# Kernel optimization log

Hardware: AMD Instinct MI355X
Metric: run time of the kernel (lower is better)

Reference implementation:

```python
import jax, jax.numpy as jnp
import numpy as np

TYPE_PANEL, TYPE_DIALOG, TYPE_CHAR = 1, 2, 3
NUM_ELEMS = 64  # max element index per type (panel count cap per page)
B, S, D = 8, 4096, 768
NPC, NDS = 4, 4  # num_panel_classes, num_dialog_shapes


def setup_inputs() -> dict:
    key = jax.random.key(0)
    ks = jax.random.split(key, 16)
    w = lambda k, shp: jax.random.normal(k, shp, dtype=jnp.float32) * 0.02
    return {
        "element_types": jax.random.randint(ks[0], (B, S), 0, 4, dtype=jnp.int32),
        "element_indices": jax.random.randint(ks[1], (B, S), 0, NUM_ELEMS, dtype=jnp.int32),
        "parent_panel_indices": jax.random.randint(ks[2], (B, S), 0, NUM_ELEMS, dtype=jnp.int32),
        "style_vector": jax.random.normal(ks[3], (B, 4), dtype=jnp.float32),
        "type_emb": w(ks[4], (4, D)),
        "index_emb": w(ks[5], (NUM_ELEMS, D)),
        "parent_emb": w(ks[6], (NUM_ELEMS, D)),
        "style_w": w(ks[7], (4, D)),
        "style_b": jnp.zeros((D,), jnp.float32),
        "ln_g": jnp.ones((D,), jnp.float32),
        "ln_b": jnp.zeros((D,), jnp.float32),
        "panel_w": w(ks[8], (D, NPC + 4)),
        "panel_b": jnp.zeros((NPC + 4,), jnp.float32),
        "dialog_w": w(ks[9], (2 * D, NDS + 4)),
        "dialog_b": jnp.zeros((NDS + 4,), jnp.float32),
        "char_w": w(ks[10], (2 * D, 4)),
        "char_b": jnp.zeros((4,), jnp.float32),
    }


def reference(element_types, element_indices, parent_panel_indices, style_vector,
              type_emb, index_emb, parent_emb, style_w, style_b, ln_g, ln_b,
              panel_w, panel_b, dialog_w, dialog_b, char_w, char_b):
    Bv, Sv = element_types.shape
    # --- TokenLayoutEncoder: embedding sum + style projection + LayerNorm ---
    x = type_emb[element_types] + index_emb[element_indices] + parent_emb[parent_panel_indices]
    x = x + (style_vector @ style_w + style_b)[:, None, :]
    mu = x.mean(-1, keepdims=True)
    var = ((x - mu) ** 2).mean(-1, keepdims=True)
    feats = (x - mu) * jax.lax.rsqrt(var + 1e-5) * ln_g + ln_b  # (B,S,D)

    # --- vectorized _build_parent_remap: orig panel idx -> kept panel order pos ---
    panel_mask = element_types == TYPE_PANEL                      # (B,S)
    kept = (jnp.cumsum(panel_mask, axis=1) - 1).astype(jnp.int32) # order pos of each panel token
    brow = jnp.arange(Bv, dtype=jnp.int32)[:, None]
    col = jnp.where(panel_mask, element_indices, NUM_ELEMS)       # dummy slot for non-panels
    remap = (jnp.full((Bv, NUM_ELEMS + 1), -1, jnp.int32)
             .at[brow, col].max(kept))[:, :NUM_ELEMS]             # (B, NUM_ELEMS)
    # kept panel order pos -> sequence position (for parent feature gather)
    slot = jnp.where(panel_mask, kept, Sv)
    seq_ids = jnp.broadcast_to(jnp.arange(Sv, dtype=jnp.int32), (Bv, Sv))
    pos_table = (jnp.zeros((Bv, Sv + 1), jnp.int32)
                 .at[brow, slot].set(seq_ids))[:, :Sv]            # (B,S)

    # --- parent_pos per token (DIALOG/CHAR only), -1 otherwise ---
    child_mask = (element_types == TYPE_DIALOG) | (element_types == TYPE_CHAR)
    ppos = jnp.where(child_mask,
                     jnp.take_along_axis(remap, parent_panel_indices, axis=1), -1)
    valid = ppos >= 0
    pseq = jnp.take_along_axis(pos_table, jnp.clip(ppos, 0, Sv - 1), axis=1)
    parent_feats = jnp.take_along_axis(feats, pseq[..., None], axis=1)
    parent_feats = parent_feats * valid[..., None].astype(feats.dtype)
    cat = jnp.concatenate([feats, parent_feats], axis=-1)         # (B,S,2D)

    # --- ParallelPredictionHeads, masked per token type ---
    panel_out = (feats @ panel_w + panel_b) * panel_mask[..., None].astype(feats.dtype)
    dmask = ((element_types == TYPE_DIALOG) & valid)[..., None].astype(feats.dtype)
    cmask = ((element_types == TYPE_CHAR) & valid)[..., None].astype(feats.dtype)
    dialog_out = (cat @ dialog_w + dialog_b) * dmask
    char_out = (cat @ char_w + char_b) * cmask
    return panel_out, dialog_out, char_out
```

## Files before the change

### kernel.cpp

```cpp
#include <hip/hip_runtime.h>

#define NB 8
#define NS 4096
#define ND 768

typedef float4 f4;

static __device__ __forceinline__ f4 ld4(const float* __restrict__ p, int i) {
    return ((const f4*)p)[i];
}

static __device__ __forceinline__ void dot4(float& acc, const f4& a, const f4& w) {
    acc = fmaf(a.x, w.x, acc);
    acc = fmaf(a.y, w.y, acc);
    acc = fmaf(a.z, w.z, acc);
    acc = fmaf(a.w, w.w, acc);
}

__global__ __launch_bounds__(256) void lp_pre(
    const int* __restrict__ et, const int* __restrict__ ei,
    const float* __restrict__ sv, const float* __restrict__ sw,
    const float* __restrict__ sb,
    const float* __restrict__ pw, const float* __restrict__ dw,
    const float* __restrict__ cw,
    int* __restrict__ table, float* __restrict__ sprj,
    float* __restrict__ pwx, float* __restrict__ dwx, float* __restrict__ cwx)
{
    const int bx = blockIdx.x;
    if (bx < 128) {
        int t = bx * 256 + threadIdx.x;
        if (et[t] == 1) {
            int b = t >> 12;
            atomicMax(&table[b * 64 + ei[t]], t & (NS - 1));
        }
    } else if (bx < 130) {
        const int lane = threadIdx.x & 63;
        const int b = (bx - 128) * 4 + (threadIdx.x >> 6);
        const float sv0 = sv[b*4+0], sv1 = sv[b*4+1], sv2 = sv[b*4+2], sv3 = sv[b*4+3];
        #pragma unroll
        for (int g = 0; g < 3; ++g) {
            int i = g*64 + lane;
            f4 w0 = ld4(sw, i), w1 = ld4(sw, 192+i), w2 = ld4(sw, 384+i), w3 = ld4(sw, 576+i);
            f4 bb = ld4(sb, i);
            f4 r;
            r.x = bb.x + sv0*w0.x + sv1*w1.x + sv2*w2.x + sv3*w3.x;
            r.y = bb.y + sv0*w0.y + sv1*w1.y + sv2*w2.y + sv3*w3.y;
            r.z = bb.z + sv0*w0.z + sv1*w1.z + sv2*w2.z + sv3*w3.z;
            r.w = bb.w + sv0*w0.w + sv1*w1.w + sv2*w2.w + sv3*w3.w;
            ((f4*)(sprj + b*ND))[i] = r;
        }
    } else {
        const int q = (bx - 130) * 256 + threadIdx.x;
        f4 r;
        if (q < 1536) {
            int o = q / 192, i = q - o * 192, d0 = 4 * i;
            r.x = pw[(d0+0)*8 + o];
            r.y = pw[(d0+1)*8 + o];
            r.z = pw[(d0+2)*8 + o];
            r.w = pw[(d0+3)*8 + o];
            ((f4*)pwx)[q] = r;
        } else if (q < 4608) {
            int u = q - 1536;
            int o = u / 384, i = u - o * 384;
            int d0 = (i < 192) ? 4*i : 768 + 4*(i - 192);
            r.x = dw[(d0+0)*8 + o];
            r.y = dw[(d0+1)*8 + o];
            r.z = dw[(d0+2)*8 + o];
            r.w = dw[(d0+3)*8 + o];
            ((f4*)dwx)[u] = r;
        } else {
            int u = q - 4608;
            int o = u / 384, i = u - o * 384;
            int d0 = (i < 192) ? 4*i : 768 + 4*(i - 192);
            r.x = cw[(d0+0)*4 + o];
            r.y = cw[(d0+1)*4 + o];
            r.z = cw[(d0+2)*4 + o];
            r.w = cw[(d0+3)*4 + o];
            ((f4*)cwx)[u] = r;
        }
    }
}

__global__ __launch_bounds__(256) void lp_main(
    const int* __restrict__ et, const int* __restrict__ ei, const int* __restrict__ ppi,
    const float* __restrict__ temb, const float* __restrict__ iemb,
    const float* __restrict__ pemb, const float* __restrict__ lng,
    const float* __restrict__ lnb,
    const float* __restrict__ pb, const float* __restrict__ db,
    const float* __restrict__ cb,
    const int* __restrict__ table, const float* __restrict__ sprj,
    const float* __restrict__ pwx, const float* __restrict__ dwx,
    const float* __restrict__ cwx,
    float* __restrict__ out)
{
    const int lane = threadIdx.x & 63;
    const int t = blockIdx.x * 4 + (threadIdx.x >> 6);
    const int b = t >> 12;
    const int type = et[t];

    f4 z4; z4.x = 0.f; z4.y = 0.f; z4.z = 0.f; z4.w = 0.f;
    f4 po0 = z4, po1 = z4, dq0 = z4, dq1 = z4, cq0 = z4;

    if (type != 0) {
        const int my_ei = ei[t], my_ppi = ppi[t];
        const int pp = table[b * 64 + my_ppi];
        const int ptokc = b * NS + (pp > 0 ? pp : 0);
        const int pei = ei[ptokc], pppi = ppi[ptokc];

        const float* te = temb + type * ND;
        const float* ie = iemb + my_ei * ND;
        const float* pe = pemb + my_ppi * ND;
        const float* sp = sprj + b * ND;

        f4 x[3], xs[3];
        float s1 = 0.f, sq = 0.f;
        #pragma unroll
        for (int g = 0; g < 3; ++g) {
            int i = g * 64 + lane;
            f4 a = ld4(te, i), c = ld4(ie, i), d = ld4(pe, i), s = ld4(sp, i);
            xs[g] = s;
            f4 v;
            v.x = a.x + c.x + d.x + s.x;
            v.y = a.y + c.y + d.y + s.y;
            v.z = a.z + c.z + d.z + s.z;
            v.w = a.w + c.w + d.w + s.w;
            x[g] = v;
            s1 += v.x + v.y + v.z + v.w;
            sq = fmaf(v.x, v.x, sq);
            sq = fmaf(v.y, v.y, sq);
            sq = fmaf(v.z, v.z, sq);
            sq = fmaf(v.w, v.w, sq);
        }

        if (type == 1) {
            #pragma unroll
            for (int k = 32; k >= 1; k >>= 1) {
                s1 += __shfl_xor(s1, k, 64);
                sq += __shfl_xor(sq, k, 64);
            }
            float mu = s1 * (1.f / ND);
            float rs = rsqrtf(sq * (1.f / ND) - mu * mu + 1e-5f);
            float c0 = -mu * rs;
            #pragma unroll
            for (int g = 0; g < 3; ++g) {
                int i = g * 64 + lane;
                f4 gg = ld4(lng, i), bb = ld4(lnb, i);
                f4 v = x[g], xn;
                xn.x = fmaf(v.x, rs, c0); v.x = fmaf(xn.x, gg.x, bb.x);
                xn.y = fmaf(v.y, rs, c0); v.y = fmaf(xn.y, gg.y, bb.y);
                xn.z = fmaf(v.z, rs, c0); v.z = fmaf(xn.z, gg.z, bb.z);
                xn.w = fmaf(v.w, rs, c0); v.w = fmaf(xn.w, gg.w, bb.w);
                x[g] = v;
            }
            float acc[8];
            #pragma unroll
            for (int o = 0; o < 8; ++o) acc[o] = 0.f;
            #pragma unroll
            for (int g = 0; g < 3; ++g) {
                int i = g * 64 + lane;
                #pragma unroll
                for (int o = 0; o < 8; ++o)
                    dot4(acc[o], x[g], ld4(pwx, o * 192 + i));
            }
            #pragma unroll
            for (int k = 32; k >= 1; k >>= 1) {
                #pragma unroll
                for (int o = 0; o < 8; ++o)
                    acc[o] += __shfl_xor(acc[o], k, 64);
            }
            po0.x = acc[0] + pb[0]; po0.y = acc[1] + pb[1];
            po0.z = acc[2] + pb[2]; po0.w = acc[3] + pb[3];
            po1.x = acc[4] + pb[4]; po1.y = acc[5] + pb[5];
            po1.z = acc[6] + pb[6]; po1.w = acc[7] + pb[7];
        } else if (pp >= 0) {
            const float* ie2 = iemb + pei * ND;
            const float* pe2 = pemb + pppi * ND;
            f4 xp[3];
            float s1p = 0.f, sqp = 0.f;
            #pragma unroll
            for (int g = 0; g < 3; ++g) {
                int i = g * 64 + lane;
                f4 a = ld4(temb + ND, i), c = ld4(ie2, i), d = ld4(pe2, i);
                f4 v;
                v.x = a.x + c.x + d.x + xs[g].x;
                v.y = a.y + c.y + d.y + xs[g].y;
                v.z = a.z + c.z + d.z + xs[g].z;
                v.w = a.w + c.w + d.w + xs[g].w;
                xp[g] = v;
                s1p += v.x + v.y + v.z + v.w;
                sqp = fmaf(v.x, v.x, sqp);
                sqp = fmaf(v.y, v.y, sqp);
                sqp = fmaf(v.z, v.z, sqp);
                sqp = fmaf(v.w, v.w, sqp);
            }
            #pragma unroll
            for (int k = 32; k >= 1; k >>= 1) {
                s1  += __shfl_xor(s1,  k, 64);
                sq  += __shfl_xor(sq,  k, 64);
                s1p += __shfl_xor(s1p, k, 64);
                sqp += __shfl_xor(sqp, k, 64);
            }
            float mu  = s1  * (1.f / ND);
            float rs  = rsqrtf(sq  * (1.f / ND) - mu  * mu  + 1e-5f);
            float mup = s1p * (1.f / ND);
            float rsp = rsqrtf(sqp * (1.f / ND) - mup * mup + 1e-5f);
            float c0 = -mu * rs, c0p = -mup * rsp;
            #pragma unroll
            for (int g = 0; g < 3; ++g) {
                int i = g * 64 + lane;
                f4 gg = ld4(lng, i), bb = ld4(lnb, i);
                f4 v = x[g], w = xp[g], xn;
                xn.x = fmaf(v.x, rs, c0); v.x = fmaf(xn.x, gg.x, bb.x);
                xn.y = fmaf(v.y, rs, c0); v.y = fmaf(xn.y, gg.y, bb.y);
                xn.z = fmaf(v.z, rs, c0); v.z = fmaf(xn.z, gg.z, bb.z);
                xn.w = fmaf(v.w, rs, c0); v.w = fmaf(xn.w, gg.w, bb.w);
                x[g] = v;
                xn.x = fmaf(w.x, rsp, c0p); w.x = fmaf(xn.x, gg.x, bb.x);
                xn.y = fmaf(w.y, rsp, c0p); w.y = fmaf(xn.y, gg.y, bb.y);
                xn.z = fmaf(w.z, rsp, c0p); w.z = fmaf(xn.z, gg.z, bb.z);
                xn.w = fmaf(w.w, rsp, c0p); w.w = fmaf(xn.w, gg.w, bb.w);
                xp[g] = w;
            }
            if (type == 2) {
                float acc[8];
                #pragma unroll
                for (int o = 0; o < 8; ++o) acc[o] = 0.f;
                #pragma unroll
                for (int g = 0; g < 3; ++g) {
                    int i = g * 64 + lane;
                    #pragma unroll
                    for (int o = 0; o < 8; ++o) {
                        dot4(acc[o], x[g],  ld4(dwx, o * 384 + i));
                        dot4(acc[o], xp[g], ld4(dwx, o * 384 + 192 + i));
                    }
                }
                #pragma unroll
                for (int k = 32; k >= 1; k >>= 1) {
                    #pragma unroll
                    for (int o = 0; o < 8; ++o)
                        acc[o] += __shfl_xor(acc[o], k, 64);
                }
                dq0.x = acc[0] + db[0]; dq0.y = acc[1] + db[1];
                dq0.z = acc[2] + db[2]; dq0.w = acc[3] + db[3];
                dq1.x = acc[4] + db[4]; dq1.y = acc[5] + db[5];
                dq1.z = acc[6] + db[6]; dq1.w = acc[7] + db[7];
            } else {
                float acc[4];
                #pragma unroll
                for (int o = 0; o < 4; ++o) acc[o] = 0.f;
                #pragma unroll
                for (int g = 0; g < 3; ++g) {
                    int i = g * 64 + lane;
                    #pragma unroll
                    for (int o = 0; o < 4; ++o) {
                        dot4(acc[o], x[g],  ld4(cwx, o * 384 + i));
                        dot4(acc[o], xp[g], ld4(cwx, o * 384 + 192 + i));
                    }
                }
                #pragma unroll
                for (int k = 32; k >= 1; k >>= 1) {
                    #pragma unroll
                    for (int o = 0; o < 4; ++o)
                        acc[o] += __shfl_xor(acc[o], k, 64);
                }
                cq0.x = acc[0] + cb[0]; cq0.y = acc[1] + cb[1];
                cq0.z = acc[2] + cb[2]; cq0.w = acc[3] + cb[3];
            }
        }
    }

    if (lane == 0) {
        f4* op = (f4*)(out + (size_t)t * 8);
        op[0] = po0; op[1] = po1;
        f4* od = (f4*)(out + (size_t)NB * NS * 8 + (size_t)t * 8);
        od[0] = dq0; od[1] = dq1;
        ((f4*)(out + (size_t)NB * NS * 16 + (size_t)t * 4))[0] = cq0;
    }
}

extern "C" void kernel_launch(void* const* d_in, const int* in_sizes, int n_in,
                              void* d_out, int out_size, void* d_ws, size_t ws_size,
                              hipStream_t stream) {
    const int* et  = (const int*)d_in[0];
    const int* ei  = (const int*)d_in[1];
    const int* ppi = (const int*)d_in[2];
    const float* sv   = (const float*)d_in[3];
    const float* temb = (const float*)d_in[4];
    const float* iemb = (const float*)d_in[5];
    const float* pemb = (const float*)d_in[6];
    const float* sw   = (const float*)d_in[7];
    const float* sb   = (const float*)d_in[8];
    const float* lng  = (const float*)d_in[9];
    const float* lnb  = (const float*)d_in[10];
    const float* pw   = (const float*)d_in[11];
    const float* pb   = (const float*)d_in[12];
    const float* dw   = (const float*)d_in[13];
    const float* db   = (const float*)d_in[14];
    const float* cw   = (const float*)d_in[15];
    const float* cbp  = (const float*)d_in[16];
    float* out = (float*)d_out;

    int*   table = (int*)d_ws;
    float* sprj  = (float*)((char*)d_ws + 4096);
    float* pwx   = (float*)((char*)d_ws + 32768);
    float* dwx   = (float*)((char*)d_ws + 32768 + 24576);
    float* cwx   = (float*)((char*)d_ws + 32768 + 24576 + 49152);

    hipMemsetAsync(table, 0xFF, NB * 64 * sizeof(int), stream);

    lp_pre<<<154, 256, 0, stream>>>(et, ei, sv, sw, sb, pw, dw, cw,
                                    table, sprj, pwx, dwx, cwx);
    lp_main<<<(NB*NS)/4, 256, 0, stream>>>(et, ei, ppi, temb, iemb, pemb,
                                           lng, lnb, pb, db, cbp,
                                           table, sprj, pwx, dwx, cwx, out);
}
```

Before: 149.8 us.

## Precompute normalized parent-panel features once per slot in a separate kernel

Adds an lp_parent kernel that computes the LayerNorm'd feature of each kept panel slot (B*64 rows) into a workspace buffer. Dialog and character tokens then read that precomputed row instead of regathering and renormalizing their parent's embeddings. This removes redundant per-token parent LayerNorm work and lowers register pressure, which it exploits by adding a launch_bounds occupancy hint of 8. The cost is an extra kernel launch and a global round trip for the parent features.

```diff
diff --git a/kernel.cpp b/kernel.cpp
--- a/kernel.cpp
+++ b/kernel.cpp
@@ -81,7 +81,65 @@
     }
 }
 
-__global__ __launch_bounds__(256) void lp_main(
+__global__ __launch_bounds__(256) void lp_parent(
+    const int* __restrict__ ei, const int* __restrict__ ppi,
+    const float* __restrict__ temb, const float* __restrict__ iemb,
+    const float* __restrict__ pemb, const float* __restrict__ lng,
+    const float* __restrict__ lnb,
+    const int* __restrict__ table, const float* __restrict__ sprj,
+    float* __restrict__ pfeat)
+{
+    const int lane = threadIdx.x & 63;
+    const int slot = blockIdx.x * 4 + (threadIdx.x >> 6);
+    const int b = slot >> 6;
+    const int pp = table[slot];
+    if (pp < 0) return;
+    const int ptok = b * NS + pp;
+    const int pei = ei[ptok], pppi = ppi[ptok];
+    const float* ie = iemb + pei * ND;
+    const float* pe = pemb + pppi * ND;
+    const float* sp = sprj + b * ND;
+
+    f4 x[3]; float s1 = 0.f, sq = 0.f;
+    #pragma unroll
+    for (int g = 0; g < 3; ++g) {
+        int i = g*64 + lane;
+        f4 a = ld4(temb + ND, i), c = ld4(ie, i), d = ld4(pe, i), s = ld4(sp, i);
+        f4 v;
+        v.x = a.x + c.x + d.x + s.x;
+        v.y = a.y + c.y + d.y + s.y;
+        v.z = a.z + c.z + d.z + s.z;
+        v.w = a.w + c.w + d.w + s.w;
+        x[g] = v;
+        s1 += v.x + v.y + v.z + v.w;
+        sq = fmaf(v.x, v.x, sq);
+        sq = fmaf(v.y, v.y, sq);
+        sq = fmaf(v.z, v.z, sq);
+        sq = fmaf(v.w, v.w, sq);
+    }
+    #pragma unroll
+    for (int k = 32; k >= 1; k >>= 1) {
+        s1 += __shfl_xor(s1, k, 64);
+        sq += __shfl_xor(sq, k, 64);
+    }
+    float mu = s1 * (1.f/ND);
+    float rs = rsqrtf(sq * (1.f/ND) - mu * mu + 1e-5f);
+    float c0 = -mu * rs;
+    float* dst = pfeat + (size_t)slot * ND;
+    #pragma unroll
+    for (int g = 0; g < 3; ++g) {
+        int i = g*64 + lane;
+        f4 gg = ld4(lng, i), bb = ld4(lnb, i);
+        f4 v = x[g], xn;
+        xn.x = fmaf(v.x, rs, c0); v.x = fmaf(xn.x, gg.x, bb.x);
+        xn.y = fmaf(v.y, rs, c0); v.y = fmaf(xn.y, gg.y, bb.y);
+        xn.z = fmaf(v.z, rs, c0); v.z = fmaf(xn.z, gg.z, bb.z);
+        xn.w = fmaf(v.w, rs, c0); v.w = fmaf(xn.w, gg.w, bb.w);
+        ((f4*)dst)[i] = v;
+    }
+}
+
+__global__ __launch_bounds__(256, 8) void lp_main(
     const int* __restrict__ et, const int* __restrict__ ei, const int* __restrict__ ppi,
     const float* __restrict__ temb, const float* __restrict__ iemb,
     const float* __restrict__ pemb, const float* __restrict__ lng,
@@ -90,7 +148,7 @@
     const float* __restrict__ cb,
     const int* __restrict__ table, const float* __restrict__ sprj,
     const float* __restrict__ pwx, const float* __restrict__ dwx,
-    const float* __restrict__ cwx,
+    const float* __restrict__ cwx, const float* __restrict__ pfeat,
     float* __restrict__ out)
 {
     const int lane = threadIdx.x & 63;
@@ -103,22 +161,20 @@
 
     if (type != 0) {
         const int my_ei = ei[t], my_ppi = ppi[t];
-        const int pp = table[b * 64 + my_ppi];
-        const int ptokc = b * NS + (pp > 0 ? pp : 0);
-        const int pei = ei[ptokc], pppi = ppi[ptokc];
+        int pp = -1;
+        if (type != 1) pp = table[b * 64 + my_ppi];
 
         const float* te = temb + type * ND;
         const float* ie = iemb + my_ei * ND;
         const float* pe = pemb + my_ppi * ND;
         const float* sp = sprj + b * ND;
 
-        f4 x[3], xs[3];
+        f4 x[3];
         float s1 = 0.f, sq = 0.f;
         #pragma unroll
         for (int g = 0; g < 3; ++g) {
             int i = g * 64 + lane;
             f4 a = ld4(te, i), c = ld4(ie, i), d = ld4(pe, i), s = ld4(sp, i);
-            xs[g] = s;
             f4 v;
             v.x = a.x + c.x + d.x + s.x;
             v.y = a.y + c.y + d.y + s.y;
@@ -131,27 +187,27 @@
             sq = fmaf(v.z, v.z, sq);
             sq = fmaf(v.w, v.w, sq);
         }
+        #pragma unroll
+        for (int k = 32; k >= 1; k >>= 1) {
+            s1 += __shfl_xor(s1, k, 64);
+            sq += __shfl_xor(sq, k, 64);
+        }
+        float mu = s1 * (1.f / ND);
+        float rs = rsqrtf(sq * (1.f / ND) - mu * mu + 1e-5f);
+        float c0 = -mu * rs;
+        #pragma unroll
+        for (int g = 0; g < 3; ++g) {
+            int i = g * 64 + lane;
+            f4 gg = ld4(lng, i), bb = ld4(lnb, i);
+            f4 v = x[g], xn;
+            xn.x = fmaf(v.x, rs, c0); v.x = fmaf(xn.x, gg.x, bb.x);
+            xn.y = fmaf(v.y, rs, c0); v.y = fmaf(xn.y, gg.y, bb.y);
+            xn.z = fmaf(v.z, rs, c0); v.z = fmaf(xn.z, gg.z, bb.z);
+            xn.w = fmaf(v.w, rs, c0); v.w = fmaf(xn.w, gg.w, bb.w);
+            x[g] = v;
+        }
 
         if (type == 1) {
-            #pragma unroll
-            for (int k = 32; k >= 1; k >>= 1) {
-                s1 += __shfl_xor(s1, k, 64);
-                sq += __shfl_xor(sq, k, 64);
-            }
-            float mu = s1 * (1.f / ND);
-            float rs = rsqrtf(sq * (1.f / ND) - mu * mu + 1e-5f);
-            float c0 = -mu * rs;
-            #pragma unroll
-            for (int g = 0; g < 3; ++g) {
-                int i = g * 64 + lane;
-                f4 gg = ld4(lng, i), bb = ld4(lnb, i);
-                f4 v = x[g], xn;
-                xn.x = fmaf(v.x, rs, c0); v.x = fmaf(xn.x, gg.x, bb.x);
-                xn.y = fmaf(v.y, rs, c0); v.y = fmaf(xn.y, gg.y, bb.y);
-                xn.z = fmaf(v.z, rs, c0); v.z = fmaf(xn.z, gg.z, bb.z);
-                xn.w = fmaf(v.w, rs, c0); v.w = fmaf(xn.w, gg.w, bb.w);
-                x[g] = v;
-            }
             float acc[8];
             #pragma unroll
             for (int o = 0; o < 8; ++o) acc[o] = 0.f;
@@ -159,8 +215,11 @@
             for (int g = 0; g < 3; ++g) {
                 int i = g * 64 + lane;
                 #pragma unroll
-                for (int o = 0; o < 8; ++o)
-                    dot4(acc[o], x[g], ld4(pwx, o * 192 + i));
+                for (int oq = 0; oq < 2; ++oq) {
+                    #pragma unroll
+                    for (int o = 0; o < 4; ++o)
+                        dot4(acc[oq*4+o], x[g], ld4(pwx, (oq*4+o) * 192 + i));
+                }
             }
             #pragma unroll
             for (int k = 32; k >= 1; k >>= 1) {
@@ -173,54 +232,7 @@
             po1.x = acc[4] + pb[4]; po1.y = acc[5] + pb[5];
             po1.z = acc[6] + pb[6]; po1.w = acc[7] + pb[7];
         } else if (pp >= 0) {
-            const float* ie2 = iemb + pei * ND;
-            const float* pe2 = pemb + pppi * ND;
-            f4 xp[3];
-            float s1p = 0.f, sqp = 0.f;
-            #pragma unroll
-            for (int g = 0; g < 3; ++g) {
-                int i = g * 64 + lane;
-                f4 a = ld4(temb + ND, i), c = ld4(ie2, i), d = ld4(pe2, i);
-                f4 v;
-                v.x = a.x + c.x + d.x + xs[g].x;
-                v.y = a.y + c.y + d.y + xs[g].y;
-                v.z = a.z + c.z + d.z + xs[g].z;
-                v.w = a.w + c.w + d.w + xs[g].w;
-                xp[g] = v;
-                s1p += v.x + v.y + v.z + v.w;
-                sqp = fmaf(v.x, v.x, sqp);
-                sqp = fmaf(v.y, v.y, sqp);
-                sqp = fmaf(v.z, v.z, sqp);
-                sqp = fmaf(v.w, v.w, sqp);
-            }
-            #pragma unroll
-            for (int k = 32; k >= 1; k >>= 1) {
-                s1  += __shfl_xor(s1,  k, 64);
-                sq  += __shfl_xor(sq,  k, 64);
-                s1p += __shfl_xor(s1p, k, 64);
-                sqp += __shfl_xor(sqp, k, 64);
-            }
-            float mu  = s1  * (1.f / ND);
-            float rs  = rsqrtf(sq  * (1.f / ND) - mu  * mu  + 1e-5f);
-            float mup = s1p * (1.f / ND);
-            float rsp = rsqrtf(sqp * (1.f / ND) - mup * mup + 1e-5f);
-            float c0 = -mu * rs, c0p = -mup * rsp;
-            #pragma unroll
-            for (int g = 0; g < 3; ++g) {
-                int i = g * 64 + lane;
-                f4 gg = ld4(lng, i), bb = ld4(lnb, i);
-                f4 v = x[g], w = xp[g], xn;
-                xn.x = fmaf(v.x, rs, c0); v.x = fmaf(xn.x, gg.x, bb.x);
-                xn.y = fmaf(v.y, rs, c0); v.y = fmaf(xn.y, gg.y, bb.y);
-                xn.z = fmaf(v.z, rs, c0); v.z = fmaf(xn.z, gg.z, bb.z);
-                xn.w = fmaf(v.w, rs, c0); v.w = fmaf(xn.w, gg.w, bb.w);
-                x[g] = v;
-                xn.x = fmaf(w.x, rsp, c0p); w.x = fmaf(xn.x, gg.x, bb.x);
-                xn.y = fmaf(w.y, rsp, c0p); w.y = fmaf(xn.y, gg.y, bb.y);
-                xn.z = fmaf(w.z, rsp, c0p); w.z = fmaf(xn.z, gg.z, bb.z);
-                xn.w = fmaf(w.w, rsp, c0p); w.w = fmaf(xn.w, gg.w, bb.w);
-                xp[g] = w;
-            }
+            const float* pfr = pfeat + (size_t)(b * 64 + my_ppi) * ND;
             if (type == 2) {
                 float acc[8];
                 #pragma unroll
@@ -229,9 +241,23 @@
                 for (int g = 0; g < 3; ++g) {
                     int i = g * 64 + lane;
                     #pragma unroll
-                    for (int o = 0; o < 8; ++o) {
-                        dot4(acc[o], x[g],  ld4(dwx, o * 384 + i));
-                        dot4(acc[o], xp[g], ld4(dwx, o * 384 + 192 + i));
+                    for (int oq = 0; oq < 2; ++oq) {
+                        #pragma unroll
+                        for (int o = 0; o < 4; ++o)
+                            dot4(acc[oq*4+o], x[g], ld4(dwx, (oq*4+o) * 384 + i));
+                    }
+                }
+                #pragma unroll
+                for (int g = 0; g < 3; ++g)
+                    x[g] = ld4(pfr, g * 64 + lane);
+                #pragma unroll
+                for (int g = 0; g < 3; ++g) {
+                    int i = g * 64 + lane;
+                    #pragma unroll
+                    for (int oq = 0; oq < 2; ++oq) {
+                        #pragma unroll
+                        for (int o = 0; o < 4; ++o)
+                            dot4(acc[oq*4+o], x[g], ld4(dwx, (oq*4+o) * 384 + 192 + i));
                     }
                 }
                 #pragma unroll
@@ -252,10 +278,18 @@
                 for (int g = 0; g < 3; ++g) {
                     int i = g * 64 + lane;
                     #pragma unroll
-                    for (int o = 0; o < 4; ++o) {
-                        dot4(acc[o], x[g],  ld4(cwx, o * 384 + i));
-                        dot4(acc[o], xp[g], ld4(cwx, o * 384 + 192 + i));
-                    }
+                    for (int o = 0; o < 4; ++o)
+                        dot4(acc[o], x[g], ld4(cwx, o * 384 + i));
+                }
+                #pragma unroll
+                for (int g = 0; g < 3; ++g)
+                    x[g] = ld4(pfr, g * 64 + lane);
+                #pragma unroll
+                for (int g = 0; g < 3; ++g) {
+                    int i = g * 64 + lane;
+                    #pragma unroll
+                    for (int o = 0; o < 4; ++o)
+                        dot4(acc[o], x[g], ld4(cwx, o * 384 + 192 + i));
                 }
                 #pragma unroll
                 for (int k = 32; k >= 1; k >>= 1) {
@@ -305,12 +339,16 @@
     float* pwx   = (float*)((char*)d_ws + 32768);
     float* dwx   = (float*)((char*)d_ws + 32768 + 24576);
     float* cwx   = (float*)((char*)d_ws + 32768 + 24576 + 49152);
+    float* pfeat = (float*)((char*)d_ws + 32768 + 24576 + 49152 + 24576);
 
     hipMemsetAsync(table, 0xFF, NB * 64 * sizeof(int), stream);
 
     lp_pre<<<154, 256, 0, stream>>>(et, ei, sv, sw, sb, pw, dw, cw,
                                     table, sprj, pwx, dwx, cwx);
+    lp_parent<<<128, 256, 0, stream>>>(ei, ppi, temb, iemb, pemb, lng, lnb,
+                                       table, sprj, pfeat);
     lp_main<<<(NB*NS)/4, 256, 0, stream>>>(et, ei, ppi, temb, iemb, pemb,
                                            lng, lnb, pb, db, cbp,
-                                           table, sprj, pwx, dwx, cwx, out);
-}
+                                           table, sprj, pwx, dwx, cwx, pfeat,
+                                           out);
+}
```

New measurement: 171.3 us. 14.3% more time.
